# Optimization experiments

Measured on AMD Instinct MI355X. Metric: run time of the kernel, lower is better.

## Reference

```python
import jax, jax.numpy as jnp
import numpy as np

THRESHOLD = 1.0  # snntorch Leaky default threshold
BETA = 0.9
ATAN_ALPHA = 2.0  # snntorch surrogate.atan default alpha

# Heaviside forward with ATan surrogate gradient (snntorch surrogate.atan)
@jax.custom_vjp
def atan_spike(x):
    return (x > 0).astype(x.dtype)

def _atan_fwd(x):
    return atan_spike(x), x

def _atan_bwd(x, g):
    # d/dx ~ (alpha/2) / (1 + (pi/2 * alpha * x)^2)
    return (g * (ATAN_ALPHA / 2.0) / (1.0 + (jnp.pi / 2.0 * ATAN_ALPHA * x) ** 2),)

atan_spike.defvjp(_atan_fwd, _atan_bwd)


def setup_inputs() -> dict:
    key = jax.random.key(0)
    kx, kw = jax.random.split(key)
    T, B, N_in, N_out = 128, 64, 1024, 1024
    x = (jax.random.uniform(kx, (T, B, N_in)) < 0.2).astype(jnp.float32)
    # kaiming_uniform_(mode='fan_in', nonlinearity='tanh'): gain=5/3, bound=gain*sqrt(3/fan_in)
    bound = (5.0 / 3.0) * np.sqrt(3.0 / N_in)
    W = jax.random.uniform(kw, (N_out, N_in), minval=-bound, maxval=bound, dtype=jnp.float32)
    return {"x": x, "W": W}


def reference(x, W):
    # x: (T, B, N_in) -> current: (T, B, N_out) via bias-free linear (vmapped over T)
    cur = jnp.einsum('tbi,oi->tbo', x, W)
    mem0 = jnp.zeros(cur.shape[1:], cur.dtype)

    # snntorch Leaky (reset_mechanism='subtract'):
    #   reset_t = detached spike of previous mem; mem_t = beta*mem_{t-1} + I_t - reset_t*thr
    #   spk_t = fire(mem_t)
    def step(mem, c_t):
        reset = jax.lax.stop_gradient(atan_spike(mem - THRESHOLD))
        mem_new = BETA * mem + c_t - reset * THRESHOLD
        spk = atan_spike(mem_new - THRESHOLD)
        return mem_new, (spk, mem_new)

    _, (spk_rec, mem_rec) = jax.lax.scan(step, mem0, cur)
    return spk_rec, mem_rec
```

## Files before the change

### kernel.cpp

```cpp
#include <hip/hip_runtime.h>
#include <cstddef>

constexpr int T_STEPS = 128;
constexpr int BATCH   = 64;
constexpr int N_IN    = 1024;
constexpr int N_OUT   = 1024;
constexpr int M_TOTAL = T_STEPS * BATCH;
constexpr int NEURONS = BATCH * N_OUT;
constexpr int OUT_HALF = T_STEPS * NEURONS;

constexpr double W_SCALE     = 17179869184.0;
constexpr double W_INV_SCALE = 1.0 / 17179869184.0;

typedef int i32x4 __attribute__((ext_vector_type(4)));

__global__ __launch_bounds__(256)
void prep_all(const float* __restrict__ x, const float* __restrict__ W,
              signed char* __restrict__ xi8, signed char* __restrict__ pi8)
{
    const int bid = blockIdx.x;
    if (bid < 2048) {
        const int i = bid * 256 + threadIdx.x;
        const float4 a = ((const float4*)x)[4 * i + 0];
        const float4 b = ((const float4*)x)[4 * i + 1];
        const float4 c = ((const float4*)x)[4 * i + 2];
        const float4 d = ((const float4*)x)[4 * i + 3];
        const float f[16] = {a.x,a.y,a.z,a.w, b.x,b.y,b.z,b.w,
                             c.x,c.y,c.z,c.w, d.x,d.y,d.z,d.w};
        union { signed char b[16]; int4 v; } u;
#pragma unroll
        for (int j = 0; j < 16; ++j) u.b[j] = (signed char)(f[j] != 0.0f);
        ((int4*)xi8)[i] = u.v;
    } else {
        const int i = (bid - 2048) * 256 + threadIdx.x;
        const float4 wv = ((const float4*)W)[i];
        const float wf[4] = {wv.x, wv.y, wv.z, wv.w};
        union { signed char b[4]; unsigned u; } dig[4];
#pragma unroll
        for (int j = 0; j < 4; ++j) {
            int q = __double2int_rn((double)wf[j] * W_SCALE);
            const int d0 = ((q + 128) & 255) - 128;  q = (q - d0) >> 8;
            const int d1 = ((q + 128) & 255) - 128;  q = (q - d1) >> 8;
            const int d2 = ((q + 128) & 255) - 128;  q = (q - d2) >> 8;
            dig[0].b[j] = (signed char)d0;
            dig[1].b[j] = (signed char)d1;
            dig[2].b[j] = (signed char)d2;
            dig[3].b[j] = (signed char)q;
        }
        unsigned* pw = (unsigned*)pi8;
#pragma unroll
        for (int p = 0; p < 4; ++p) pw[p * 262144 + i] = dig[p].u;
    }
}

__device__ __forceinline__ void gload_lds16(const signed char* g, signed char* l)
{
    __builtin_amdgcn_global_load_lds(
        (const __attribute__((address_space(1))) unsigned*)(g),
        (__attribute__((address_space(3))) unsigned*)(l), 16, 0, 0);
}

__global__ __launch_bounds__(512)
void gemm_planes(const signed char* __restrict__ xi8, const signed char* __restrict__ pi8,
                 unsigned* __restrict__ outw)
{
    __shared__ __align__(16) signed char As[128 * 64];
    __shared__ __align__(16) signed char Bs[4 * 128 * 64];

    const int tid  = threadIdx.x;
    const int m0   = blockIdx.x * 128;
    const int n0   = blockIdx.y * 128;
    const int lane = tid & 63;
    const int w    = tid >> 6;
    const int wm   = w >> 2;
    const int wn   = w & 3;
    const int l15  = lane & 15;
    const int kg   = lane >> 4;
    const int swzr = (l15 >> 1) & 3;

    const int srow   = lane >> 2;
    const int schunk = (lane & 3) ^ ((lane >> 3) & 3);

    i32x4 acc[4][4][2] = {};

    for (int k0 = 0; k0 < N_IN; k0 += 64) {
        gload_lds16(xi8 + (size_t)(m0 + w * 16 + srow) * N_IN + k0 + schunk * 16,
                    As + w * 1024);
#pragma unroll
        for (int i = 0; i < 4; ++i) {
            const int seg  = w * 4 + i;
            const int p    = seg >> 3;
            const int rowp = (seg & 7) * 16 + srow;
            gload_lds16(pi8 + (size_t)p * 1048576 + (size_t)(n0 + rowp) * N_IN
                            + k0 + schunk * 16,
                        Bs + seg * 1024);
        }
        __syncthreads();

        i32x4 af[4], bf[2][4];
#pragma unroll
        for (int fm = 0; fm < 4; ++fm) {
            const int row = wm * 64 + fm * 16 + l15;
            af[fm] = *(const i32x4*)(As + row * 64 + (kg ^ swzr) * 16);
        }
#pragma unroll
        for (int fn = 0; fn < 2; ++fn) {
            const int row = wn * 32 + fn * 16 + l15;
#pragma unroll
            for (int p = 0; p < 4; ++p)
                bf[fn][p] = *(const i32x4*)(Bs + p * 8192 + row * 64 + (kg ^ swzr) * 16);
        }

#pragma unroll
        for (int p = 0; p < 4; ++p)
#pragma unroll
            for (int fm = 0; fm < 4; ++fm)
#pragma unroll
                for (int fn = 0; fn < 2; ++fn)
                    acc[p][fm][fn] = __builtin_amdgcn_mfma_i32_16x16x64_i8(
                        af[fm], bf[fn][p], acc[p][fm][fn], 0, 0, 0);
        __syncthreads();
    }

#pragma unroll
    for (int fm = 0; fm < 4; ++fm)
#pragma unroll
        for (int fn = 0; fn < 2; ++fn)
#pragma unroll
            for (int r = 0; r < 4; ++r) {
                const int m = m0 + wm * 64 + fm * 16 + kg * 4 + r;
                const int o = n0 + wn * 32 + fn * 16 + l15;
                const double q = (double)acc[3][fm][fn][r] * 16777216.0
                               + (double)acc[2][fm][fn][r] * 65536.0
                               + (double)acc[1][fm][fn][r] * 256.0
                               + (double)acc[0][fm][fn][r];
                const double cur = q * W_INV_SCALE;
                const unsigned long long u = (unsigned long long)__double_as_longlong(cur);
                const int t = m >> 6;
                const int b = m & 63;
                const size_t idx = (size_t)t * NEURONS + (size_t)b * N_OUT + o;
                outw[idx]            = (unsigned)u;
                outw[OUT_HALF + idx] = (unsigned)(u >> 32);
            }
}

__global__ __launch_bounds__(256)
void lif_scan(unsigned* outw)
{
    const int n = blockIdx.x * 256 + threadIdx.x;
    double mem = 0.0;
    double c[8], cn[8];
#pragma unroll
    for (int j = 0; j < 8; ++j) {
        const size_t idx = (size_t)j * NEURONS + n;
        const unsigned lo = outw[idx];
        const unsigned hi = outw[OUT_HALF + idx];
        c[j] = __longlong_as_double((long long)(((unsigned long long)hi << 32) | lo));
    }
    for (int t0 = 0; t0 < T_STEPS; t0 += 8) {
        if (t0 + 8 < T_STEPS) {
#pragma unroll
            for (int j = 0; j < 8; ++j) {
                const size_t idx = (size_t)(t0 + 8 + j) * NEURONS + n;
                const unsigned lo = outw[idx];
                const unsigned hi = outw[OUT_HALF + idx];
                cn[j] = __longlong_as_double((long long)(((unsigned long long)hi << 32) | lo));
            }
        }
#pragma unroll
        for (int j = 0; j < 8; ++j) {
            const double reset = (mem > 1.0) ? 1.0 : 0.0;
            mem = 0.9 * mem + c[j] - reset;
            const size_t idx = (size_t)(t0 + j) * NEURONS + n;
            outw[idx]            = (mem > 1.0) ? 0x3f800000u : 0u;
            outw[OUT_HALF + idx] = __float_as_uint((float)mem);
        }
#pragma unroll
        for (int j = 0; j < 8; ++j) c[j] = cn[j];
    }
}

extern "C" void kernel_launch(void* const* d_in, const int* in_sizes, int n_in,
                              void* d_out, int out_size, void* d_ws, size_t ws_size,
                              hipStream_t stream)
{
    const float* x = (const float*)d_in[0];
    const float* W = (const float*)d_in[1];
    unsigned* outw = (unsigned*)d_out;

    signed char* xi8 = (signed char*)d_ws;
    signed char* pi8 = xi8 + (size_t)M_TOTAL * N_IN;

    prep_all<<<3072, 256, 0, stream>>>(x, W, xi8, pi8);

    dim3 ggrid(M_TOTAL / 128, N_OUT / 128);
    gemm_planes<<<ggrid, 512, 0, stream>>>(xi8, pi8, outw);

    lif_scan<<<NEURONS / 256, 256, 0, stream>>>(outw);
}
```

Measured before the change: 161.4 us.

## Fuse GEMM with LIF scan by tiling over all timesteps per batch row

```diff
diff --git a/kernel.cpp b/kernel.cpp
--- a/kernel.cpp
+++ b/kernel.cpp
@@ -61,15 +61,17 @@
 }
 
 __global__ __launch_bounds__(512)
-void gemm_planes(const signed char* __restrict__ xi8, const signed char* __restrict__ pi8,
-                 unsigned* __restrict__ outw)
+void gemm_lif(const signed char* __restrict__ xi8, const signed char* __restrict__ pi8,
+              unsigned* __restrict__ outw)
 {
-    __shared__ __align__(16) signed char As[128 * 64];
-    __shared__ __align__(16) signed char Bs[4 * 128 * 64];
+    __shared__ __align__(16) unsigned char smem[128 * 66 * 8];
+    signed char* As = (signed char*)smem;
+    signed char* Bs = (signed char*)smem + 8192;
+    double (*curL)[66] = (double (*)[66])smem;
 
     const int tid  = threadIdx.x;
-    const int m0   = blockIdx.x * 128;
-    const int n0   = blockIdx.y * 128;
+    const int b    = blockIdx.y;
+    const int o0   = blockIdx.x * 64;
     const int lane = tid & 63;
     const int w    = tid >> 6;
     const int wm   = w >> 2;
@@ -81,102 +83,81 @@
     const int srow   = lane >> 2;
     const int schunk = (lane & 3) ^ ((lane >> 3) & 3);
 
-    i32x4 acc[4][4][2] = {};
+    i32x4 acc[4][4] = {};
 
     for (int k0 = 0; k0 < N_IN; k0 += 64) {
-        gload_lds16(xi8 + (size_t)(m0 + w * 16 + srow) * N_IN + k0 + schunk * 16,
+        gload_lds16(xi8 + (size_t)((w * 16 + srow) * 64 + b) * N_IN + k0 + schunk * 16,
                     As + w * 1024);
 #pragma unroll
-        for (int i = 0; i < 4; ++i) {
-            const int seg  = w * 4 + i;
-            const int p    = seg >> 3;
-            const int rowp = (seg & 7) * 16 + srow;
-            gload_lds16(pi8 + (size_t)p * 1048576 + (size_t)(n0 + rowp) * N_IN
+        for (int i = 0; i < 2; ++i) {
+            const int seg  = w * 2 + i;
+            const int p    = seg >> 2;
+            const int rowp = (seg & 3) * 16 + srow;
+            gload_lds16(pi8 + (size_t)p * 1048576 + (size_t)(o0 + rowp) * N_IN
                             + k0 + schunk * 16,
                         Bs + seg * 1024);
         }
         __syncthreads();
 
-        i32x4 af[4], bf[2][4];
+        i32x4 af[4], bf[4];
 #pragma unroll
         for (int fm = 0; fm < 4; ++fm) {
             const int row = wm * 64 + fm * 16 + l15;
             af[fm] = *(const i32x4*)(As + row * 64 + (kg ^ swzr) * 16);
         }
-#pragma unroll
-        for (int fn = 0; fn < 2; ++fn) {
-            const int row = wn * 32 + fn * 16 + l15;
+        {
+            const int row = wn * 16 + l15;
 #pragma unroll
             for (int p = 0; p < 4; ++p)
-                bf[fn][p] = *(const i32x4*)(Bs + p * 8192 + row * 64 + (kg ^ swzr) * 16);
+                bf[p] = *(const i32x4*)(Bs + p * 4096 + row * 64 + (kg ^ swzr) * 16);
         }
 
 #pragma unroll
         for (int p = 0; p < 4; ++p)
 #pragma unroll
             for (int fm = 0; fm < 4; ++fm)
-#pragma unroll
-                for (int fn = 0; fn < 2; ++fn)
-                    acc[p][fm][fn] = __builtin_amdgcn_mfma_i32_16x16x64_i8(
-                        af[fm], bf[fn][p], acc[p][fm][fn], 0, 0, 0);
+                acc[p][fm] = __builtin_amdgcn_mfma_i32_16x16x64_i8(
+                    af[fm], bf[p], acc[p][fm], 0, 0, 0);
         __syncthreads();
     }
 
+    const int onl = wn * 16 + l15;
 #pragma unroll
     for (int fm = 0; fm < 4; ++fm)
 #pragma unroll
-        for (int fn = 0; fn < 2; ++fn)
+        for (int r = 0; r < 4; ++r) {
+            const int t = wm * 64 + fm * 16 + kg * 4 + r;
+            const double q = (double)acc[3][fm][r] * 16777216.0
+                           + (double)acc[2][fm][r] * 65536.0
+                           + (double)acc[1][fm][r] * 256.0
+                           + (double)acc[0][fm][r];
+            curL[t][onl] = q * W_INV_SCALE;
+        }
+    __syncthreads();
+
+    if (tid < 64) {
+        const int oc = tid;
+        const size_t nbase = (size_t)b * N_OUT + o0 + oc;
+        double mem = 0.0;
+        double c[8], cn[8];
 #pragma unroll
-            for (int r = 0; r < 4; ++r) {
-                const int m = m0 + wm * 64 + fm * 16 + kg * 4 + r;
-                const int o = n0 + wn * 32 + fn * 16 + l15;
-                const double q = (double)acc[3][fm][fn][r] * 16777216.0
-                               + (double)acc[2][fm][fn][r] * 65536.0
-                               + (double)acc[1][fm][fn][r] * 256.0
-                               + (double)acc[0][fm][fn][r];
-                const double cur = q * W_INV_SCALE;
-                const unsigned long long u = (unsigned long long)__double_as_longlong(cur);
-                const int t = m >> 6;
-                const int b = m & 63;
-                const size_t idx = (size_t)t * NEURONS + (size_t)b * N_OUT + o;
-                outw[idx]            = (unsigned)u;
-                outw[OUT_HALF + idx] = (unsigned)(u >> 32);
+        for (int j = 0; j < 8; ++j) c[j] = curL[j][oc];
+        for (int t0 = 0; t0 < T_STEPS; t0 += 8) {
+            if (t0 + 8 < T_STEPS) {
+#pragma unroll
+                for (int j = 0; j < 8; ++j) cn[j] = curL[t0 + 8 + j][oc];
             }
-}
-
-__global__ __launch_bounds__(256)
-void lif_scan(unsigned* outw)
-{
-    const int n = blockIdx.x * 256 + threadIdx.x;
-    double mem = 0.0;
-    double c[8], cn[8];
-#pragma unroll
-    for (int j = 0; j < 8; ++j) {
-        const size_t idx = (size_t)j * NEURONS + n;
-        const unsigned lo = outw[idx];
-        const unsigned hi = outw[OUT_HALF + idx];
-        c[j] = __longlong_as_double((long long)(((unsigned long long)hi << 32) | lo));
-    }
-    for (int t0 = 0; t0 < T_STEPS; t0 += 8) {
-        if (t0 + 8 < T_STEPS) {
 #pragma unroll
             for (int j = 0; j < 8; ++j) {
-                const size_t idx = (size_t)(t0 + 8 + j) * NEURONS + n;
-                const unsigned lo = outw[idx];
-                const unsigned hi = outw[OUT_HALF + idx];
-                cn[j] = __longlong_as_double((long long)(((unsigned long long)hi << 32) | lo));
+                const double reset = (mem > 1.0) ? 1.0 : 0.0;
+                mem = 0.9 * mem + c[j] - reset;
+                const size_t idx = (size_t)(t0 + j) * NEURONS + nbase;
+                outw[idx]            = (mem > 1.0) ? 0x3f800000u : 0u;
+                outw[OUT_HALF + idx] = __float_as_uint((float)mem);
             }
+#pragma unroll
+            for (int j = 0; j < 8; ++j) c[j] = cn[j];
         }
-#pragma unroll
-        for (int j = 0; j < 8; ++j) {
-            const double reset = (mem > 1.0) ? 1.0 : 0.0;
-            mem = 0.9 * mem + c[j] - reset;
-            const size_t idx = (size_t)(t0 + j) * NEURONS + n;
-            outw[idx]            = (mem > 1.0) ? 0x3f800000u : 0u;
-            outw[OUT_HALF + idx] = __float_as_uint((float)mem);
-        }
-#pragma unroll
-        for (int j = 0; j < 8; ++j) c[j] = cn[j];
     }
 }
 
@@ -193,8 +174,6 @@
 
     prep_all<<<3072, 256, 0, stream>>>(x, W, xi8, pi8);
 
-    dim3 ggrid(M_TOTAL / 128, N_OUT / 128);
-    gemm_planes<<<ggrid, 512, 0, stream>>>(xi8, pi8, outw);
-
-    lif_scan<<<NEURONS / 256, 256, 0, stream>>>(outw);
+    dim3 ggrid(N_OUT / 64, BATCH);
+    gemm_lif<<<ggrid, 512, 0, stream>>>(xi8, pi8, outw);
 }
```

Result: faster. 132.4 us (-18.0%).
